# Performance work log

Measured on AMD Instinct MI355X. Metric: run time of the kernel, lower is better.

## Reference

```python
import jax, jax.numpy as jnp
import numpy as np

B, C, HS, WS = 2, 256, 64, 64
NH, DK, DV = 2, 128, 128
EPS = 1e-6


def setup_inputs() -> dict:
    key = jax.random.key(0)
    ks = jax.random.split(key, 8)
    s = 0.02
    return {
        "x": jax.random.normal(ks[0], (B, C, HS, WS), jnp.float32),
        "Wq": jax.random.normal(ks[1], (NH, DK, C), jnp.float32) * s,
        "bq": jnp.zeros((NH, DK), jnp.float32),
        "Wk": jax.random.normal(ks[2], (NH, DK, C), jnp.float32) * s,
        "bk": jnp.zeros((NH, DK), jnp.float32),
        "Wv": jax.random.normal(ks[3], (NH, DV, C), jnp.float32) * s,
        "bv": jnp.zeros((NH, DV), jnp.float32),
        "scale": jnp.ones((NH,), jnp.float32),  # softmax_scale per head (l2scaled)
        "Wm": jax.random.normal(ks[4], (C, NH * DV), jnp.float32) * s,
        "bm": jnp.zeros((C,), jnp.float32),
    }


def _l2norm(t):
    # F.normalize along channel dim (axis=2 of [B,H,dk,L]) with eps=1e-6
    n = jnp.sqrt(jnp.sum(t * t, axis=2, keepdims=True))
    return t / jnp.maximum(n, EPS)


def reference(x, Wq, bq, Wk, bk, Wv, bv, scale, Wm, bm):
    b, c, h, w = x.shape
    L = h * w
    xf = x.reshape(b, c, L)                               # [B,C,L]
    # 1x1 conv QKV projections (per head)
    Q = jnp.einsum('hkc,bcl->bhkl', Wq, xf) + bq[None, :, :, None]
    K = jnp.einsum('hkc,bcl->bhkl', Wk, xf) + bk[None, :, :, None]
    V = jnp.einsum('hvc,bcl->bhvl', Wv, xf) + bv[None, :, :, None]
    # l2scaled QK-normalization: cosine similarity with learned scale
    sc = jnp.sqrt(scale)[None, :, None, None]             # scale**0.5 per head
    Qn = _l2norm(Q) * sc
    Kn = _l2norm(K) * sc
    # attention over spatial tokens: [B,H,L,L]
    A = jax.nn.softmax(jnp.einsum('bhkl,bhkm->bhlm', Qn, Kn), axis=-1)
    R = jnp.einsum('bhlm,bhvm->bhvl', A, V)               # [B,H,dv,L]
    R = R.reshape(b, NH * DV, L)                          # concat heads on channels
    out = jnp.einsum('oc,bcl->bol', Wm, R) + bm[None, :, None]  # 1x1 merge conv
    out = out.reshape(b, c, h, w)
    return out + x                                        # residual (nnd op is identity)
```

## Files before the change

kernel.cpp:

```cpp
#include <hip/hip_runtime.h>


#define BB  2
#define CC  256
#define LL  4096
#define NHD 2
#define DKD 128
#define DVD 128

#define QBLK   64
#define KVBLK  64
#define SPLITK 2
#define TPS    (LL / SPLITK / KVBLK)

typedef short  short8  __attribute__((ext_vector_type(8)));
typedef float  f32x4   __attribute__((ext_vector_type(4)));
typedef unsigned short ushort4v __attribute__((ext_vector_type(4)));

__device__ __forceinline__ unsigned short f2bf(float f) {
  union { float f; unsigned u; } v; v.f = f;
  unsigned r = v.u + 0x7fffu + ((v.u >> 16) & 1u);
  return (unsigned short)(r >> 16);
}
__device__ __forceinline__ float bf2f(unsigned short u) {
  union { unsigned u; float f; } v; v.u = ((unsigned)u) << 16;
  return v.f;
}
__device__ __forceinline__ void glds16(const unsigned short* g, unsigned short* l) {
  __builtin_amdgcn_global_load_lds(
      (const __attribute__((address_space(1))) void*)g,
      (__attribute__((address_space(3))) void*)l, 16, 0, 0);
}

__global__ __launch_bounds__(256) void mhsa_pre_kernel(
    const float* __restrict__ x,
    const float* __restrict__ Wq, const float* __restrict__ Wk,
    const float* __restrict__ Wv,
    unsigned short* __restrict__ Xt, unsigned short* __restrict__ wbf)
{
  const int z = blockIdx.z;
  if (z == 2) {
    if (blockIdx.y) return;
    int base = blockIdx.x * 1536 + threadIdx.x;
    #pragma unroll
    for (int i = 0; i < 6; ++i) {
      int idx = base + i * 256;
      int p = idx >> 16;
      int rem = idx & 65535;
      const float* W = p == 0 ? Wq : (p == 1 ? Wk : Wv);
      wbf[idx] = f2bf(W[rem]);
    }
    return;
  }
  const int b  = z;
  const int l0 = blockIdx.x * 32, c0 = blockIdx.y * 32;
  __shared__ float Ts[32][33];
  const int tid = threadIdx.x;
  const int tl  = tid & 31, tc = tid >> 5;
  const float* xb = x + (size_t)b * CC * LL;
  #pragma unroll
  for (int pp = 0; pp < 4; ++pp) {
    int c = tc + pp * 8;
    Ts[c][tl] = xb[(size_t)(c0 + c) * LL + l0 + tl];
  }
  __syncthreads();
  unsigned short* Xb = Xt + (size_t)b * LL * CC;
  #pragma unroll
  for (int pp = 0; pp < 4; ++pp) {
    int l = tc + pp * 8;
    Xb[(size_t)(l0 + l) * CC + c0 + tl] = f2bf(Ts[tl][l]);
  }
}

__global__ __launch_bounds__(256) void mhsa_projm_kernel(
    const unsigned short* __restrict__ Xt,
    const unsigned short* __restrict__ wbf,
    const float* __restrict__ bq, const float* __restrict__ bk,
    const float* __restrict__ bv, const float* __restrict__ scale,
    unsigned short* __restrict__ qn, unsigned short* __restrict__ kn,
    unsigned short* __restrict__ vb)
{
  const int lt0 = blockIdx.x * 64;
  const int bh  = blockIdx.y;
  const int p   = blockIdx.z;
  const int h   = bh & 1, b = bh >> 1;

  const unsigned short* W = wbf + ((size_t)p * 2 + h) * (128 * 256);
  const unsigned short* X = Xt + (size_t)b * LL * CC;
  const float* bias = (p == 0 ? bq : (p == 1 ? bk : bv)) + h * 128;

  __shared__ unsigned short Ws[2][128 * 64];
  __shared__ unsigned short Xs[2][64 * 64];
  __shared__ float red[4][64];

  const int wave = threadIdx.x >> 6;
  const int lane = threadIdx.x & 63;
  const int lr = lane & 15, lc = lane >> 4;

  int offW[4], ldsW[4], offX[2], ldsX[2];
  #pragma unroll
  for (int j = 0; j < 4; ++j) {
    int ii = wave * 4 + j;
    int r  = ii * 8 + (lane >> 3);
    int c  = (lane & 7) ^ (lane >> 3);
    offW[j] = r * 256 + c * 8;
    ldsW[j] = ii * 512;
  }
  #pragma unroll
  for (int j = 0; j < 2; ++j) {
    int ii = wave * 2 + j;
    int r  = ii * 8 + (lane >> 3);
    int c  = (lane & 7) ^ (lane >> 3);
    offX[j] = (lt0 + r) * 256 + c * 8;
    ldsX[j] = ii * 512;
  }

  f32x4 acc[2][4];
  #pragma unroll
  for (int kt2 = 0; kt2 < 2; ++kt2)
    #pragma unroll
    for (int lt = 0; lt < 4; ++lt) acc[kt2][lt] = (f32x4){0.f, 0.f, 0.f, 0.f};

  #pragma unroll
  for (int j = 0; j < 4; ++j) glds16(W + offW[j], &Ws[0][ldsW[j]]);
  #pragma unroll
  for (int j = 0; j < 2; ++j) glds16(X + offX[j], &Xs[0][ldsX[j]]);
  __syncthreads();

  const int sw = lr & 7;
  int buf = 0;
  for (int step = 0; step < 4; ++step) {
    if (step < 3) {
      int c0 = (step + 1) * 64;
      #pragma unroll
      for (int j = 0; j < 4; ++j) glds16(W + c0 + offW[j], &Ws[buf ^ 1][ldsW[j]]);
      #pragma unroll
      for (int j = 0; j < 2; ++j) glds16(X + c0 + offX[j], &Xs[buf ^ 1][ldsX[j]]);
    }
    #pragma unroll
    for (int ks = 0; ks < 2; ++ks) {
      short8 af[2], bf_[4];
      #pragma unroll
      for (int kt2 = 0; kt2 < 2; ++kt2)
        af[kt2] = *reinterpret_cast<const short8*>(
            &Ws[buf][(wave * 32 + kt2 * 16 + lr) * 64 + ((ks * 4 + lc) ^ sw) * 8]);
      #pragma unroll
      for (int lt = 0; lt < 4; ++lt)
        bf_[lt] = *reinterpret_cast<const short8*>(
            &Xs[buf][(lt * 16 + lr) * 64 + ((ks * 4 + lc) ^ sw) * 8]);
      #pragma unroll
      for (int kt2 = 0; kt2 < 2; ++kt2)
        #pragma unroll
        for (int lt = 0; lt < 4; ++lt)
          acc[kt2][lt] = __builtin_amdgcn_mfma_f32_16x16x32_bf16(
              af[kt2], bf_[lt], acc[kt2][lt], 0, 0, 0);
    }
    __syncthreads();
    buf ^= 1;
  }

  #pragma unroll
  for (int kt2 = 0; kt2 < 2; ++kt2)
    #pragma unroll
    for (int r = 0; r < 4; ++r) {
      float bsv = bias[wave * 32 + kt2 * 16 + lc * 4 + r];
      #pragma unroll
      for (int lt = 0; lt < 4; ++lt) acc[kt2][lt][r] += bsv;
    }

  if (p < 2) {
    float s[4];
    #pragma unroll
    for (int lt = 0; lt < 4; ++lt) {
      float v = 0.f;
      #pragma unroll
      for (int kt2 = 0; kt2 < 2; ++kt2)
        #pragma unroll
        for (int r = 0; r < 4; ++r) v += acc[kt2][lt][r] * acc[kt2][lt][r];
      v += __shfl_xor(v, 16, 64);
      v += __shfl_xor(v, 32, 64);
      s[lt] = v;
    }
    if (lc == 0) {
      #pragma unroll
      for (int lt = 0; lt < 4; ++lt) red[wave][lt * 16 + lr] = s[lt];
    }
    __syncthreads();
    float sq = sqrtf(scale[h]);
    unsigned short* out = (p == 0 ? qn : kn) + (size_t)bh * LL * DKD;
    #pragma unroll
    for (int lt = 0; lt < 4; ++lt) {
      int l = lt * 16 + lr;
      float sum = red[0][l] + red[1][l] + red[2][l] + red[3][l];
      float nv = sq / fmaxf(sqrtf(sum), 1e-6f);
      #pragma unroll
      for (int kt2 = 0; kt2 < 2; ++kt2) {
        ushort4v pk;
        #pragma unroll
        for (int r = 0; r < 4; ++r) pk[r] = f2bf(acc[kt2][lt][r] * nv);
        *reinterpret_cast<ushort4v*>(
            out + (size_t)(lt0 + l) * DKD + wave * 32 + kt2 * 16 + lc * 4) = pk;
      }
    }
  } else {
    unsigned short* outv = vb + (size_t)bh * DVD * LL;
    #pragma unroll
    for (int kt2 = 0; kt2 < 2; ++kt2)
      #pragma unroll
      for (int r = 0; r < 4; ++r)
        #pragma unroll
        for (int lt = 0; lt < 4; ++lt)
          outv[(size_t)(wave * 32 + kt2 * 16 + lc * 4 + r) * LL + lt0 + lt * 16 + lr]
              = f2bf(acc[kt2][lt][r]);
  }
}

__global__ __launch_bounds__(256) void mhsa_attn_kernel(
    const unsigned short* __restrict__ qn,
    const unsigned short* __restrict__ kn,
    const unsigned short* __restrict__ vb,
    const float* __restrict__ scale,
    unsigned short* __restrict__ pr,
    float* __restrict__ ls)
{
  const int wgid = (blockIdx.z * gridDim.y + blockIdx.y) * gridDim.x + blockIdx.x;
  const int xcd  = wgid & 7;
  const int slot = wgid >> 3;
  const int bh   = xcd >> 1;
  const int qt   = ((xcd & 1) << 5) | (slot & 31);
  const int s    = slot >> 5;
  const int l0   = qt * QBLK;
  const int kbase = s * (LL / SPLITK);

  const int wave = threadIdx.x >> 6;
  const int lane = threadIdx.x & 63;
  const int lr   = lane & 15;
  const int lc   = lane >> 4;

  const unsigned short* Q = qn + (size_t)bh * LL * DKD;
  const unsigned short* K = kn + (size_t)bh * LL * DKD;
  const unsigned short* V = vb + (size_t)bh * DVD * LL;
  const float M = scale[bh & 1];

  __shared__ unsigned short Ks[2][KVBLK * DKD];
  __shared__ unsigned short Vs[2][DVD * KVBLK];
  __shared__ unsigned short plds[4][16 * 72];
  unsigned short* myp = plds[wave];

  const int l0w = l0 + wave * 16;
  short8 qf[4];
  #pragma unroll
  for (int ks = 0; ks < 4; ++ks)
    qf[ks] = *reinterpret_cast<const short8*>(Q + (size_t)(l0w + lr) * DKD + ks * 32 + lc * 8);

  int offK[4], offV[4], ldsOff[4];
  #pragma unroll
  for (int j = 0; j < 4; ++j) {
    int ii = wave * 4 + j;
    int rK = ii * 4 + (lane >> 4);
    int cK = (lane & 15) ^ (rK & 7);
    offK[j] = rK * DKD + cK * 8;
    int vV = ii * 8 + (lane >> 3);
    int cV = (lane & 7) ^ (lane >> 3);
    offV[j] = vV * LL + cV * 8;
    ldsOff[j] = ii * 512;
  }

  f32x4 racc[8];
  #pragma unroll
  for (int vt = 0; vt < 8; ++vt) racc[vt] = (f32x4){0.f, 0.f, 0.f, 0.f};
  float lsum[4] = {0.f, 0.f, 0.f, 0.f};

  #pragma unroll
  for (int j = 0; j < 4; ++j) {
    glds16(K + (size_t)kbase * DKD + offK[j], &Ks[0][ldsOff[j]]);
    glds16(V + kbase + offV[j],               &Vs[0][ldsOff[j]]);
  }
  __syncthreads();

  const int sw = lr & 7;
  int buf = 0;
  for (int t = 0; t < TPS; ++t) {
    if (t + 1 < TPS) {
      int m1 = kbase + (t + 1) * KVBLK;
      #pragma unroll
      for (int j = 0; j < 4; ++j) {
        glds16(K + (size_t)m1 * DKD + offK[j], &Ks[buf ^ 1][ldsOff[j]]);
        glds16(V + m1 + offV[j],               &Vs[buf ^ 1][ldsOff[j]]);
      }
    }

    f32x4 sx[4];
    #pragma unroll
    for (int ct = 0; ct < 4; ++ct) {
      f32x4 acc = (f32x4){0.f, 0.f, 0.f, 0.f};
      #pragma unroll
      for (int ks = 0; ks < 4; ++ks) {
        short8 kf = *reinterpret_cast<const short8*>(
            &Ks[buf][(ct * 16 + lr) * DKD + ((ks * 4 + lc) ^ sw) * 8]);
        acc = __builtin_amdgcn_mfma_f32_16x16x32_bf16(qf[ks], kf, acc, 0, 0, 0);
      }
      sx[ct] = acc;
    }

    #pragma unroll
    for (int ct = 0; ct < 4; ++ct) {
      #pragma unroll
      for (int r = 0; r < 4; ++r) {
        float pv = __expf(sx[ct][r] - M);
        sx[ct][r] = pv;
        lsum[r] += pv;
      }
    }

    #pragma unroll
    for (int ct = 0; ct < 4; ++ct)
      #pragma unroll
      for (int r = 0; r < 4; ++r)
        myp[(lc * 4 + r) * 72 + ct * 16 + lr] = f2bf(sx[ct][r]);

    short8 pf[2];
    #pragma unroll
    for (int ks = 0; ks < 2; ++ks)
      pf[ks] = *reinterpret_cast<const short8*>(&myp[lr * 72 + ks * 32 + lc * 8]);

    #pragma unroll
    for (int vt = 0; vt < 8; ++vt) {
      #pragma unroll
      for (int ks = 0; ks < 2; ++ks) {
        short8 vf = *reinterpret_cast<const short8*>(
            &Vs[buf][(vt * 16 + lr) * KVBLK + ((ks * 4 + lc) ^ sw) * 8]);
        racc[vt] = __builtin_amdgcn_mfma_f32_16x16x32_bf16(pf[ks], vf, racc[vt], 0, 0, 0);
      }
    }

    __syncthreads();
    buf ^= 1;
  }

  #pragma unroll
  for (int r = 0; r < 4; ++r) {
    float v = lsum[r];
    #pragma unroll
    for (int msk = 8; msk; msk >>= 1) v += __shfl_xor(v, msk, 64);
    lsum[r] = v;
  }
  if (lr == 0) {
    #pragma unroll
    for (int r = 0; r < 4; ++r)
      ls[((size_t)s * 4 + bh) * LL + l0w + lc * 4 + r] = lsum[r];
  }

  unsigned short* Pb = pr + ((size_t)s * 4 + bh) * DVD * LL;
  #pragma unroll
  for (int vt = 0; vt < 8; ++vt) {
    ushort4v pk;
    #pragma unroll
    for (int r = 0; r < 4; ++r) pk[r] = f2bf(racc[vt][r]);
    *reinterpret_cast<ushort4v*>(Pb + (size_t)(vt * 16 + lr) * LL + l0w + lc * 4) = pk;
  }
}

__global__ __launch_bounds__(256) void mhsa_merge_kernel(
    const unsigned short* __restrict__ pr,
    const float* __restrict__ ls,
    const float* __restrict__ Wm,
    const float* __restrict__ bm,
    const float* __restrict__ x,
    float* __restrict__ out)
{
  const int l0 = blockIdx.x * 64;
  const int o0 = blockIdx.y * 64;
  const int b  = blockIdx.z;

  __shared__ float WmT[32][68];
  __shared__ float Rs[32][68];
  __shared__ float invL[2][64];

  const int tid = threadIdx.x;
  const int to  = tid >> 4;
  const int tl  = tid & 15;

  if (tid < 128) {
    int h = tid >> 6, l = tid & 63;
    size_t bhl = (size_t)(b * NHD + h) * LL + l0 + l;
    float s0 = ls[bhl];
    float s1 = ls[(size_t)4 * LL + bhl];
    invL[h][l] = 1.f / (s0 + s1);
  }

  float acc[4][4];
  #pragma unroll
  for (int r = 0; r < 4; ++r)
    #pragma unroll
    for (int j = 0; j < 4; ++j) acc[r][j] = 0.f;

  const size_t sstride = (size_t)4 * DVD * LL;

  for (int c0 = 0; c0 < CC; c0 += 32) {
    __syncthreads();
    #pragma unroll
    for (int i = 0; i < 8; ++i) {
      int flat = tid + 256 * i;
      int o = flat >> 5, c = flat & 31;
      WmT[c][o] = Wm[(size_t)(o0 + o) * CC + c0 + c];
    }
    #pragma unroll
    for (int i = 0; i < 8; ++i) {
      int flat = tid + 256 * i;
      int c = flat >> 6, l = flat & 63;
      int ch = c0 + c;
      int hh = ch >> 7, v = ch & 127;
      size_t idx = ((size_t)(b * NHD + hh) * DVD + v) * LL + l0 + l;
      Rs[c][l] = (bf2f(pr[idx]) + bf2f(pr[sstride + idx])) * invL[hh][l];
    }
    __syncthreads();
    #pragma unroll 4
    for (int cc = 0; cc < 32; ++cc) {
      f32x4 wv = *(const f32x4*)&WmT[cc][to * 4];
      f32x4 rv = *(const f32x4*)&Rs[cc][tl * 4];
      #pragma unroll
      for (int r = 0; r < 4; ++r)
        #pragma unroll
        for (int j = 0; j < 4; ++j) acc[r][j] += wv[r] * rv[j];
    }
  }

  #pragma unroll
  for (int r = 0; r < 4; ++r) {
    int o = o0 + to * 4 + r;
    float bias = bm[o];
    size_t off = ((size_t)b * CC + o) * LL + l0 + tl * 4;
    f32x4 xv = *reinterpret_cast<const f32x4*>(x + off);
    f32x4 ov;
    #pragma unroll
    for (int j = 0; j < 4; ++j) ov[j] = acc[r][j] + bias + xv[j];
    *reinterpret_cast<f32x4*>(out + off) = ov;
  }
}

extern "C" void kernel_launch(void* const* d_in, const int* in_sizes, int n_in,
                              void* d_out, int out_size, void* d_ws, size_t ws_size,
                              hipStream_t stream) {
  const float* x     = (const float*)d_in[0];
  const float* Wq    = (const float*)d_in[1];
  const float* bq    = (const float*)d_in[2];
  const float* Wk    = (const float*)d_in[3];
  const float* bk    = (const float*)d_in[4];
  const float* Wv    = (const float*)d_in[5];
  const float* bv    = (const float*)d_in[6];
  const float* scale = (const float*)d_in[7];
  const float* Wm    = (const float*)d_in[8];
  const float* bm    = (const float*)d_in[9];
  float* out = (float*)d_out;

  const size_t nqk = (size_t)BB * NHD * LL * DKD;
  const size_t npr = (size_t)SPLITK * BB * NHD * DVD * LL;
  unsigned short* qn = (unsigned short*)d_ws;
  unsigned short* kn = qn + nqk;
  unsigned short* vb = kn + nqk;
  unsigned short* pr = vb + nqk;
  float* lsw = (float*)(pr + npr);
  unsigned short* Xt  = pr;
  unsigned short* wbf = pr + (size_t)BB * LL * CC;

  mhsa_pre_kernel<<<dim3(128, 8, 3), dim3(256), 0, stream>>>(
      x, Wq, Wk, Wv, Xt, wbf);
  mhsa_projm_kernel<<<dim3(LL / 64, BB * NHD, 3), dim3(256), 0, stream>>>(
      Xt, wbf, bq, bk, bv, scale, qn, kn, vb);
  mhsa_attn_kernel<<<dim3(LL / QBLK, BB * NHD, SPLITK), dim3(256), 0, stream>>>(
      qn, kn, vb, scale, pr, lsw);
  mhsa_merge_kernel<<<dim3(LL / 64, CC / 64, BB), dim3(256), 0, stream>>>(
      pr, lsw, Wm, bm, x, out);
}
```

Before: 104.5 us.

## Split merge into combine/transpose pass and bf16 MFMA merge GEMM

The fp32 scalar-FMA merge kernel is replaced by two kernels. The first combines the split-K partial results, normalises them by the softmax denominators and writes a transposed bf16 R tensor. The second runs the Wm projection as a bf16 MFMA GEMM with double-buffered, swizzled LDS loads via global_load_lds, and Wm is converted to bf16 in the pre kernel. This removes the slow scalar GEMM at the cost of an extra launch, an extra round trip through memory for R, and bf16 rounding of R and Wm.

Result: faster. 95.49 us (-8.6%).

```diff
diff --git a/kernel.cpp b/kernel.cpp
--- a/kernel.cpp
+++ b/kernel.cpp
@@ -35,20 +35,25 @@
 __global__ __launch_bounds__(256) void mhsa_pre_kernel(
     const float* __restrict__ x,
     const float* __restrict__ Wq, const float* __restrict__ Wk,
-    const float* __restrict__ Wv,
-    unsigned short* __restrict__ Xt, unsigned short* __restrict__ wbf)
+    const float* __restrict__ Wv, const float* __restrict__ Wm,
+    unsigned short* __restrict__ Xt, unsigned short* __restrict__ wbf,
+    unsigned short* __restrict__ wmb)
 {
   const int z = blockIdx.z;
   if (z == 2) {
     if (blockIdx.y) return;
-    int base = blockIdx.x * 1536 + threadIdx.x;
-    #pragma unroll
-    for (int i = 0; i < 6; ++i) {
+    int base = blockIdx.x * 2048 + threadIdx.x;
+    #pragma unroll
+    for (int i = 0; i < 8; ++i) {
       int idx = base + i * 256;
-      int p = idx >> 16;
-      int rem = idx & 65535;
-      const float* W = p == 0 ? Wq : (p == 1 ? Wk : Wv);
-      wbf[idx] = f2bf(W[rem]);
+      if (idx < 196608) {
+        int p = idx >> 16;
+        int rem = idx & 65535;
+        const float* W = p == 0 ? Wq : (p == 1 ? Wk : Wv);
+        wbf[idx] = f2bf(W[rem]);
+      } else {
+        wmb[idx - 196608] = f2bf(Wm[idx - 196608]);
+      }
     }
     return;
   }
@@ -361,81 +366,141 @@
   }
 }
 
-__global__ __launch_bounds__(256) void mhsa_merge_kernel(
+__global__ __launch_bounds__(256) void mhsa_combine_kernel(
     const unsigned short* __restrict__ pr,
     const float* __restrict__ ls,
-    const float* __restrict__ Wm,
+    unsigned short* __restrict__ Rt)
+{
+  const int l0 = blockIdx.x * 32;
+  const int c0 = blockIdx.y * 32;
+  const int b  = blockIdx.z;
+  const int hh = c0 >> 7;
+
+  __shared__ float Ts[32][33];
+  __shared__ float invl[32];
+
+  const int tid = threadIdx.x;
+  const int tl  = tid & 31, tc = tid >> 5;
+
+  if (tid < 32) {
+    size_t bhl = (size_t)(b * NHD + hh) * LL + l0 + tid;
+    invl[tid] = 1.f / (ls[bhl] + ls[(size_t)4 * LL + bhl]);
+  }
+  __syncthreads();
+
+  const size_t sstride = (size_t)4 * DVD * LL;
+  #pragma unroll
+  for (int pp = 0; pp < 4; ++pp) {
+    int cl = tc + pp * 8;
+    int v  = (c0 & 127) + cl;
+    size_t idx = ((size_t)(b * NHD + hh) * DVD + v) * LL + l0 + tl;
+    Ts[cl][tl] = (bf2f(pr[idx]) + bf2f(pr[sstride + idx])) * invl[tl];
+  }
+  __syncthreads();
+
+  unsigned short* Rb = Rt + (size_t)b * LL * CC;
+  #pragma unroll
+  for (int pp = 0; pp < 4; ++pp) {
+    int ll = tc + pp * 8;
+    Rb[(size_t)(l0 + ll) * CC + c0 + tl] = f2bf(Ts[tl][ll]);
+  }
+}
+
+__global__ __launch_bounds__(256) void mhsa_mergem_kernel(
+    const unsigned short* __restrict__ Rt,
+    const unsigned short* __restrict__ wmb,
     const float* __restrict__ bm,
     const float* __restrict__ x,
     float* __restrict__ out)
 {
-  const int l0 = blockIdx.x * 64;
-  const int o0 = blockIdx.y * 64;
-  const int b  = blockIdx.z;
-
-  __shared__ float WmT[32][68];
-  __shared__ float Rs[32][68];
-  __shared__ float invL[2][64];
-
-  const int tid = threadIdx.x;
-  const int to  = tid >> 4;
-  const int tl  = tid & 15;
-
-  if (tid < 128) {
-    int h = tid >> 6, l = tid & 63;
-    size_t bhl = (size_t)(b * NHD + h) * LL + l0 + l;
-    float s0 = ls[bhl];
-    float s1 = ls[(size_t)4 * LL + bhl];
-    invL[h][l] = 1.f / (s0 + s1);
-  }
-
-  float acc[4][4];
-  #pragma unroll
-  for (int r = 0; r < 4; ++r)
-    #pragma unroll
-    for (int j = 0; j < 4; ++j) acc[r][j] = 0.f;
-
-  const size_t sstride = (size_t)4 * DVD * LL;
-
-  for (int c0 = 0; c0 < CC; c0 += 32) {
+  const int lt0 = blockIdx.x * 64;
+  const int oh  = blockIdx.y;
+  const int b   = blockIdx.z;
+
+  const unsigned short* W = wmb + (size_t)oh * 128 * 256;
+  const unsigned short* X = Rt + (size_t)b * LL * CC;
+
+  __shared__ unsigned short Ws[2][128 * 64];
+  __shared__ unsigned short Xs[2][64 * 64];
+
+  const int wave = threadIdx.x >> 6;
+  const int lane = threadIdx.x & 63;
+  const int lr = lane & 15, lc = lane >> 4;
+
+  int offW[4], ldsW[4], offX[2], ldsX[2];
+  #pragma unroll
+  for (int j = 0; j < 4; ++j) {
+    int ii = wave * 4 + j;
+    int r  = ii * 8 + (lane >> 3);
+    int c  = (lane & 7) ^ (lane >> 3);
+    offW[j] = r * 256 + c * 8;
+    ldsW[j] = ii * 512;
+  }
+  #pragma unroll
+  for (int j = 0; j < 2; ++j) {
+    int ii = wave * 2 + j;
+    int r  = ii * 8 + (lane >> 3);
+    int c  = (lane & 7) ^ (lane >> 3);
+    offX[j] = (lt0 + r) * 256 + c * 8;
+    ldsX[j] = ii * 512;
+  }
+
+  f32x4 acc[2][4];
+  #pragma unroll
+  for (int kt2 = 0; kt2 < 2; ++kt2)
+    #pragma unroll
+    for (int lt = 0; lt < 4; ++lt) acc[kt2][lt] = (f32x4){0.f, 0.f, 0.f, 0.f};
+
+  #pragma unroll
+  for (int j = 0; j < 4; ++j) glds16(W + offW[j], &Ws[0][ldsW[j]]);
+  #pragma unroll
+  for (int j = 0; j < 2; ++j) glds16(X + offX[j], &Xs[0][ldsX[j]]);
+  __syncthreads();
+
+  const int sw = lr & 7;
+  int buf = 0;
+  for (int step = 0; step < 4; ++step) {
+    if (step < 3) {
+      int c0 = (step + 1) * 64;
+      #pragma unroll
+      for (int j = 0; j < 4; ++j) glds16(W + c0 + offW[j], &Ws[buf ^ 1][ldsW[j]]);
+      #pragma unroll
+      for (int j = 0; j < 2; ++j) glds16(X + c0 + offX[j], &Xs[buf ^ 1][ldsX[j]]);
+    }
+    #pragma unroll
+    for (int ks = 0; ks < 2; ++ks) {
+      short8 af[2], bf_[4];
+      #pragma unroll
+      for (int kt2 = 0; kt2 < 2; ++kt2)
+        af[kt2] = *reinterpret_cast<const short8*>(
+            &Ws[buf][(wave * 32 + kt2 * 16 + lr) * 64 + ((ks * 4 + lc) ^ sw) * 8]);
+      #pragma unroll
+      for (int lt = 0; lt < 4; ++lt)
+        bf_[lt] = *reinterpret_cast<const short8*>(
+            &Xs[buf][(lt * 16 + lr) * 64 + ((ks * 4 + lc) ^ sw) * 8]);
+      #pragma unroll
+      for (int kt2 = 0; kt2 < 2; ++kt2)
+        #pragma unroll
+        for (int lt = 0; lt < 4; ++lt)
+          acc[kt2][lt] = __builtin_amdgcn_mfma_f32_16x16x32_bf16(
+              af[kt2], bf_[lt], acc[kt2][lt], 0, 0, 0);
+    }
     __syncthreads();
-    #pragma unroll
-    for (int i = 0; i < 8; ++i) {
-      int flat = tid + 256 * i;
-      int o = flat >> 5, c = flat & 31;
-      WmT[c][o] = Wm[(size_t)(o0 + o) * CC + c0 + c];
-    }
-    #pragma unroll
-    for (int i = 0; i < 8; ++i) {
-      int flat = tid + 256 * i;
-      int c = flat >> 6, l = flat & 63;
-      int ch = c0 + c;
-      int hh = ch >> 7, v = ch & 127;
-      size_t idx = ((size_t)(b * NHD + hh) * DVD + v) * LL + l0 + l;
-      Rs[c][l] = (bf2f(pr[idx]) + bf2f(pr[sstride + idx])) * invL[hh][l];
-    }
-    __syncthreads();
-    #pragma unroll 4
-    for (int cc = 0; cc < 32; ++cc) {
-      f32x4 wv = *(const f32x4*)&WmT[cc][to * 4];
-      f32x4 rv = *(const f32x4*)&Rs[cc][tl * 4];
-      #pragma unroll
-      for (int r = 0; r < 4; ++r)
-        #pragma unroll
-        for (int j = 0; j < 4; ++j) acc[r][j] += wv[r] * rv[j];
-    }
-  }
-
-  #pragma unroll
-  for (int r = 0; r < 4; ++r) {
-    int o = o0 + to * 4 + r;
-    float bias = bm[o];
-    size_t off = ((size_t)b * CC + o) * LL + l0 + tl * 4;
-    f32x4 xv = *reinterpret_cast<const f32x4*>(x + off);
-    f32x4 ov;
-    #pragma unroll
-    for (int j = 0; j < 4; ++j) ov[j] = acc[r][j] + bias + xv[j];
-    *reinterpret_cast<f32x4*>(out + off) = ov;
+    buf ^= 1;
+  }
+
+  #pragma unroll
+  for (int kt2 = 0; kt2 < 2; ++kt2) {
+    #pragma unroll
+    for (int r = 0; r < 4; ++r) {
+      int o = oh * 128 + wave * 32 + kt2 * 16 + lc * 4 + r;
+      float bias = bm[o];
+      #pragma unroll
+      for (int lt = 0; lt < 4; ++lt) {
+        size_t off = ((size_t)(b * CC + o)) * LL + lt0 + lt * 16 + lr;
+        out[off] = acc[kt2][lt][r] + bias + x[off];
+      }
+    }
   }
 }
 
@@ -461,15 +526,19 @@
   unsigned short* vb = kn + nqk;
   unsigned short* pr = vb + nqk;
   float* lsw = (float*)(pr + npr);
+  unsigned short* wmb = (unsigned short*)(lsw + (size_t)SPLITK * BB * NHD * LL);
   unsigned short* Xt  = pr;
   unsigned short* wbf = pr + (size_t)BB * LL * CC;
+  unsigned short* Rt  = qn;
 
   mhsa_pre_kernel<<<dim3(128, 8, 3), dim3(256), 0, stream>>>(
-      x, Wq, Wk, Wv, Xt, wbf);
+      x, Wq, Wk, Wv, Wm, Xt, wbf, wmb);
   mhsa_projm_kernel<<<dim3(LL / 64, BB * NHD, 3), dim3(256), 0, stream>>>(
       Xt, wbf, bq, bk, bv, scale, qn, kn, vb);
   mhsa_attn_kernel<<<dim3(LL / QBLK, BB * NHD, SPLITK), dim3(256), 0, stream>>>(
       qn, kn, vb, scale, pr, lsw);
-  mhsa_merge_kernel<<<dim3(LL / 64, CC / 64, BB), dim3(256), 0, stream>>>(
-      pr, lsw, Wm, bm, x, out);
-}
+  mhsa_combine_kernel<<<dim3(LL / 32, CC / 32, BB), dim3(256), 0, stream>>>(
+      pr, lsw, Rt);
+  mhsa_mergem_kernel<<<dim3(LL / 64, 2, BB), dim3(256), 0, stream>>>(
+      Rt, wmb, bm, x, out);
+}
```
